# Performance work log

Hardware: AMD Instinct MI355X
Metric: run time of the kernel (lower is better)

The kernel has to match this reference:

```python
import jax, jax.numpy as jnp
import numpy as np
import math

B, S, HID = 2, 2048, 1536
H, HD = 12, 128           # num_heads, head_dim
LAT = HID // 8            # latent_dim = 192
ROT = HD // 2             # 64, rotary applied to this half-size subspace


def _make_rotary(seq_len, dim=ROT, base=10000.0):
    # LlamaRotaryEmbedding: inv_freq over dim/2 freqs, emb = cat(sin, cos) -> [1,1,S,dim]
    inv_freq = 1.0 / (base ** (np.arange(0, dim, 2, dtype=np.float32) / dim))
    pos = np.arange(seq_len, dtype=np.float32)
    sincos = np.einsum('i,j->ij', pos, inv_freq)  # [S, dim/2]
    emb = np.concatenate([np.sin(sincos), np.cos(sincos)], axis=-1)  # [S, dim]
    return jnp.asarray(emb)[None, None, :, :]


def setup_inputs() -> dict:
    key = jax.random.key(0)
    ks = jax.random.split(key, 10)
    sd = 0.02
    return {
        'hidden_states': jax.random.normal(ks[0], (B, S, HID), jnp.float32),
        'rotary_emb': _make_rotary(S),
        'W_kv_d':  jax.random.normal(ks[1], (HID, LAT), jnp.float32) * sd,
        'W_q_d':   jax.random.normal(ks[2], (HID, LAT), jnp.float32) * sd,
        'W_k_u':   jax.random.normal(ks[3], (LAT, H * ROT), jnp.float32) * sd,
        'W_q_u':   jax.random.normal(ks[4], (LAT, H * ROT), jnp.float32) * sd,
        'W_v_u':   jax.random.normal(ks[5], (LAT, H * HD), jnp.float32) * sd,
        'W_rope_k': jax.random.normal(ks[6], (HID, HID // 2), jnp.float32) * sd,
        'W_rope_q': jax.random.normal(ks[7], (LAT, HID // 2), jnp.float32) * sd,
        'W_o':     jax.random.normal(ks[8], (HID, HID), jnp.float32) * sd,
    }


def _apply_rope(x, emb):
    # x: [B,S,H,ROT]; emb: [1,1,S,ROT] (cat of sin,cos, each ROT/2)
    half = ROT // 2
    x1, x2 = x[..., :half], x[..., half:]
    sin = emb[..., :half].transpose(0, 2, 1, 3)  # -> [1,S,1,half] to broadcast over heads
    cos = emb[..., half:].transpose(0, 2, 1, 3)
    return jnp.concatenate([x1 * cos - x2 * sin, x1 * sin + x2 * cos], axis=-1)


def reference(hidden_states, rotary_emb, W_kv_d, W_q_d, W_k_u, W_q_u, W_v_u,
              W_rope_k, W_rope_q, W_o):
    b, s, _ = hidden_states.shape
    kv_d = hidden_states @ W_kv_d                       # [B,S,LAT]
    q_d = hidden_states @ W_q_d                         # [B,S,LAT]
    k_c = (kv_d @ W_k_u).reshape(b, s, H, ROT)          # content half of K
    q_c = (q_d @ W_q_u).reshape(b, s, H, ROT)
    v = (kv_d @ W_v_u).reshape(b, s, H, HD)
    k_r = (hidden_states @ W_rope_k).reshape(b, s, H, ROT)
    q_r = (q_d @ W_rope_q).reshape(b, s, H, ROT)
    k_r = _apply_rope(k_r, rotary_emb)
    q_r = _apply_rope(q_r, rotary_emb)
    k = jnp.concatenate([k_c, k_r], axis=-1)            # [B,S,H,HD]
    q = jnp.concatenate([q_c, q_r], axis=-1)

    scores = jnp.einsum('bqhd,bkhd->bhqk', q, k) / math.sqrt(HD)
    causal = jnp.tril(jnp.ones((s, s), dtype=bool))
    scores = jnp.where(causal[None, None], scores, jnp.float32(-1e9))
    probs = jax.nn.softmax(scores, axis=-1)
    attn = jnp.einsum('bhqk,bkhd->bqhd', probs, v).reshape(b, s, HID)
    return attn @ W_o
```

## Files before the change

### kernel.cpp

```cpp
#include <hip/hip_runtime.h>
#include <hip/hip_bf16.h>

#define B_ 2
#define S_ 2048
#define HID_ 1536
#define H_ 12
#define HD_ 128
#define LAT_ 192
#define ROT_ 64
#define M_ (B_*S_)
#define NTILE_ (B_*H_*(S_/64))

typedef __hip_bfloat16 bf16;

using short8  = __attribute__((ext_vector_type(8))) short;
using short4v = __attribute__((ext_vector_type(4))) short;
using float4v = __attribute__((ext_vector_type(4))) float;

__device__ __forceinline__ unsigned short f2bf(float f) {
  __hip_bfloat16 h = __float2bfloat16(f);
  unsigned short u; __builtin_memcpy(&u, &h, 2); return u;
}

#define GLDS16(gp, lp) __builtin_amdgcn_global_load_lds( \
    (__attribute__((address_space(1))) void*)(size_t)(gp), \
    (__attribute__((address_space(3))) void*)(lp), 16, 0, 0)

__global__ __launch_bounds__(256)
void fillf_k(float* __restrict__ out, float v, int n)
{
  int i = blockIdx.x*256 + threadIdx.x;
  if (i < n) out[i] = v;
}

__global__ __launch_bounds__(256)
void packT5_k(const float* __restrict__ s0, const float* __restrict__ s1,
              const float* __restrict__ s2, const float* __restrict__ s3,
              bf16* __restrict__ d0, bf16* __restrict__ d1,
              bf16* __restrict__ d2, bf16* __restrict__ d3,
              int Kn, int N0, int N1, int N2, int N3,
              const float* __restrict__ hsrc, bf16* __restrict__ hdst)
{
  if (blockIdx.z == 4) {
    const int nblk = gridDim.x * gridDim.y;
    const int flatb = blockIdx.y * gridDim.x + blockIdx.x;
    const float4* in4 = (const float4*)hsrc;
    for (int i = flatb*256 + threadIdx.x; i < M_*HID_/4; i += nblk*256) {
      float4 v = in4[i];
      short4v o;
      o[0] = (short)f2bf(v.x); o[1] = (short)f2bf(v.y);
      o[2] = (short)f2bf(v.z); o[3] = (short)f2bf(v.w);
      *(short4v*)&hdst[i*4] = o;
    }
    return;
  }
  const float* W; bf16* Wt; int Nn;
  switch (blockIdx.z) {
    case 0:  W = s0; Wt = d0; Nn = N0; break;
    case 1:  W = s1; Wt = d1; Nn = N1; break;
    case 2:  W = s2; Wt = d2; Nn = N2; break;
    default: W = s3; Wt = d3; Nn = N3; break;
  }
  const int kb = blockIdx.x*32, nb = blockIdx.y*32;
  if (nb >= Nn) return;
  __shared__ float t[32][33];
  const int tx = threadIdx.x & 31, ty = threadIdx.x >> 5;
  #pragma unroll
  for (int i = 0; i < 4; i++)
    t[ty+8*i][tx] = W[(size_t)(kb+ty+8*i)*Nn + nb + tx];
  __syncthreads();
  #pragma unroll
  for (int i = 0; i < 4; i++)
    Wt[(size_t)(nb + ty + 8*i)*Kn + kb + tx] = __float2bfloat16(t[tx][ty+8*i]);
}

template<int CMODE, int BM>
__global__ __launch_bounds__(256)
void gemm_mfma(const bf16* __restrict__ Av, const bf16* __restrict__ Btp,
               const bf16* __restrict__ Av2, const bf16* __restrict__ Bt2,
               void* __restrict__ Cv, void* __restrict__ Cv2,
               void* __restrict__ Cv3,
               const float* __restrict__ emb, int Kn, int lda, int ldb, int ldc)
{
  constexpr int MI  = BM/32;
  constexpr int ITA = BM/32;
  __shared__ bf16 As[(size_t)BM*64];
  __shared__ bf16 Bs[128*64];

  const int tid  = threadIdx.x;
  const int lane = tid & 63;
  const int w    = tid >> 6;
  const int col  = lane & 15, quad = lane >> 4;
  const int wr   = w >> 1, wc = w & 1;
  const size_t m0 = (size_t)blockIdx.y * BM;
  const size_t n0 = (size_t)blockIdx.x * 128;

  const bf16* Abase = Av;
  const bf16* Bt    = Btp;
  size_t nrow0 = n0;
  if constexpr (CMODE == 6) {
    if ((int)n0 >= 2304) { Abase = Av2; Bt = Bt2; nrow0 = n0 - 2304; }
  }

  const bf16* bg[4];
  #pragma unroll
  for (int it = 0; it < 4; it++) {
    int c = tid + it*256, row = c >> 3, seg = c & 7;
    bg[it] = Bt + (nrow0 + row)*ldb + (size_t)((seg ^ (row & 7))*8);
  }
  const bf16* ag[ITA];
  #pragma unroll
  for (int it = 0; it < ITA; it++) {
    int c = tid + it*256, row = c >> 3, seg = c & 7;
    ag[it] = Abase + (m0 + row)*lda + (size_t)((seg ^ (row & 7))*8);
  }

  float4v acc[MI][4];
  #pragma unroll
  for (int i=0;i<MI;i++)
    #pragma unroll
    for (int j=0;j<4;j++) acc[i][j] = (float4v){0.f,0.f,0.f,0.f};

  for (int k0 = 0; k0 < Kn; k0 += 64) {
    #pragma unroll
    for (int it = 0; it < 4; it++)
      GLDS16(bg[it] + k0, Bs + (size_t)(tid + it*256)*8);
    #pragma unroll
    for (int it = 0; it < ITA; it++)
      GLDS16(ag[it] + k0, As + (size_t)(tid + it*256)*8);
    __syncthreads();

    short8 af[MI][2], bfr[4][2];
    #pragma unroll
    for (int i=0;i<MI;i++) {
      const int ar = wr*(BM/2) + i*16 + col;
      #pragma unroll
      for (int k2=0;k2<2;k2++)
        af[i][k2] = *(const short8*)&As[ar*64 + ((k2*4+quad)^(ar&7))*8];
    }
    #pragma unroll
    for (int j=0;j<4;j++) {
      const int br = wc*64 + j*16 + col;
      #pragma unroll
      for (int k2=0;k2<2;k2++)
        bfr[j][k2] = *(const short8*)&Bs[br*64 + ((k2*4+quad)^(br&7))*8];
    }

    #pragma unroll
    for (int k2=0;k2<2;k2++)
      #pragma unroll
      for (int i=0;i<MI;i++)
        #pragma unroll
        for (int j=0;j<4;j++)
          acc[i][j] = __builtin_amdgcn_mfma_f32_16x16x32_bf16(af[i][k2], bfr[j][k2], acc[i][j], 0,0,0);
    __syncthreads();
  }

  if constexpr (CMODE == 0) {
    #pragma unroll
    for (int i=0;i<MI;i++) {
      const size_t row0 = m0 + wr*(BM/2) + i*16 + quad*4;
      #pragma unroll
      for (int j=0;j<4;j++) {
        const int c = (int)n0 + wc*64 + j*16 + col;
        #pragma unroll
        for (int r=0;r<4;r++)
          ((float*)Cv)[(row0+r)*ldc + c] = acc[i][j][r];
      }
    }
    return;
  }

  if constexpr (CMODE == 5) {
    if ((int)n0 < 384) {
      #pragma unroll
      for (int i=0;i<MI;i++) {
        const size_t row0 = m0 + wr*(BM/2) + i*16 + quad*4;
        #pragma unroll
        for (int j=0;j<4;j++) {
          const int c = (int)n0 + wc*64 + j*16 + col;
          #pragma unroll
          for (int r=0;r<4;r++)
            ((bf16*)Cv)[(row0+r)*384 + c] = __float2bfloat16(acc[i][j][r]);
        }
      }
    } else {
      const int hh = (((int)n0 - 384) >> 6) + wc;
      #pragma unroll
      for (int i=0;i<MI;i++) {
        const size_t row0 = m0 + wr*(BM/2) + i*16 + quad*4;
        #pragma unroll
        for (int j=0;j<2;j++) {
          const int idim = j*16 + col;
          #pragma unroll
          for (int r=0;r<4;r++) {
            const size_t row = row0 + r;
            const int s = (int)(row & (S_-1));
            const float sn = emb[(size_t)s*ROT_ + idim];
            const float cs = emb[(size_t)s*ROT_ + 32 + idim];
            const float x1 = acc[i][j][r], x2 = acc[i][j+2][r];
            bf16* dst = (bf16*)Cv2 + (row*H_ + hh)*HD_ + 64 + idim;
            dst[0]  = __float2bfloat16(x1*cs - x2*sn);
            dst[32] = __float2bfloat16(x1*sn + x2*cs);
          }
        }
      }
    }
    return;
  }

  if ((int)n0 < 768) {
    #pragma unroll
    for (int i=0;i<MI;i++) {
      const size_t row0 = m0 + wr*(BM/2) + i*16 + quad*4;
      #pragma unroll
      for (int j=0;j<4;j++) {
        const int c = (int)n0 + wc*64 + j*16 + col;
        #pragma unroll
        for (int r=0;r<4;r++)
          ((bf16*)Cv)[(row0+r)*HID_ + (c>>6)*HD_ + (c&63)] = __float2bfloat16(acc[i][j][r]);
      }
    }
  } else if ((int)n0 < 2304) {
    #pragma unroll
    for (int i=0;i<MI;i++) {
      const size_t row0 = m0 + wr*(BM/2) + i*16 + quad*4;
      const int bb = (int)(row0 >> 11), s = (int)(row0 & (S_-1));
      #pragma unroll
      for (int j=0;j<4;j++) {
        const int cv = (int)n0 - 768 + wc*64 + j*16 + col;
        const int hh = cv >> 7, d = cv & 127;
        short4v st;
        #pragma unroll
        for (int r=0;r<4;r++) st[r] = (short)f2bf(acc[i][j][r]);
        *(short4v*)((unsigned short*)Cv2 +
            ((size_t)(bb*H_+hh)*HD_ + d)*S_ + s) = st;
      }
    }
  } else if ((int)n0 < 3072) {
    #pragma unroll
    for (int i=0;i<MI;i++) {
      const size_t row0 = m0 + wr*(BM/2) + i*16 + quad*4;
      #pragma unroll
      for (int j=0;j<4;j++) {
        const int c = (int)n0 - 2304 + wc*64 + j*16 + col;
        #pragma unroll
        for (int r=0;r<4;r++)
          ((bf16*)Cv3)[(row0+r)*HID_ + (c>>6)*HD_ + (c&63)] = __float2bfloat16(acc[i][j][r]);
      }
    }
  } else {
    const int hh = (((int)n0 - 3072) >> 6) + wc;
    #pragma unroll
    for (int i=0;i<MI;i++) {
      const size_t row0 = m0 + wr*(BM/2) + i*16 + quad*4;
      #pragma unroll
      for (int j=0;j<2;j++) {
        const int idim = j*16 + col;
        #pragma unroll
        for (int r=0;r<4;r++) {
          const size_t row = row0 + r;
          const int s = (int)(row & (S_-1));
          const float sn = emb[(size_t)s*ROT_ + idim];
          const float cs = emb[(size_t)s*ROT_ + 32 + idim];
          const float x1 = acc[i][j][r], x2 = acc[i][j+2][r];
          bf16* dst = (bf16*)Cv3 + (row*H_ + hh)*HD_ + 64 + idim;
          dst[0]  = __float2bfloat16(x1*cs - x2*sn);
          dst[32] = __float2bfloat16(x1*sn + x2*cs);
        }
      }
    }
  }
}

#define KSTR 136
#define VSTR 72
#define PSTR 72

__global__ __launch_bounds__(256)
void attn_mfma(const bf16* __restrict__ Qf, const bf16* __restrict__ Kf,
               const bf16* __restrict__ Vtg, bf16* __restrict__ at)
{
  const int p     = (int)blockIdx.x;
  const int ii    = p & 255;
  const int third = p >> 8;
  const int rank  = (third == 0) ? ii : (third == 1 ? 511 - ii : 512 + ii);
  const int qt = (S_/64 - 1) - rank/24;
  const int bh = rank % 24;
  const int h  = bh % H_, b = bh / H_;

  const int tid  = threadIdx.x;
  const int w    = tid >> 6;
  const int lane = tid & 63;
  const int col  = lane & 15;
  const int quad = lane >> 4;

  __shared__ unsigned short Ks[64*KSTR];
  __shared__ unsigned short Vt[128*VSTR];
  __shared__ unsigned short Ps[4][16*PSTR];

  const int q0w = qt*64 + w*16;

  const unsigned short* Kb = (const unsigned short*)Kf +
      ((size_t)b*S_*H_ + h)*HD_;
  const unsigned short* Vb = (const unsigned short*)Vtg +
      (size_t)(b*H_ + h)*HD_*S_;

  const unsigned short* kgp[4]; unsigned short* kdst[4];
  const unsigned short* vgp[4]; unsigned short* vdst[4];
  #pragma unroll
  for (int it = 0; it < 4; it++) {
    int c = tid + it*256;
    int key = c >> 4, doff = (c & 15)*8;
    kgp[it]  = Kb + (size_t)key*HID_ + doff;
    kdst[it] = &Ks[key*KSTR + doff];
    int d = c >> 3, kg = (c & 7)*8;
    vgp[it]  = Vb + (size_t)d*S_ + kg;
    vdst[it] = &Vt[d*VSTR + kg];
  }

  short8 qf[4];
  {
    const unsigned short* qrow = (const unsigned short*)Qf +
        ((size_t)((size_t)b*S_ + q0w + col)*H_ + h)*HD_;
    #pragma unroll
    for (int kk = 0; kk < 4; kk++)
      qf[kk] = *(const short8*)(qrow + kk*32 + quad*8);
  }

  float4v O[8];
  #pragma unroll
  for (int t=0;t<8;t++) O[t] = (float4v){0.f,0.f,0.f,0.f};
  float m_ln = -1e30f, l_ln = 0.f;

  const float scale2 = 0.08838834764831845f * 1.4426950408889634f;

  short8 kr[4], vr[4];
  #pragma unroll
  for (int it = 0; it < 4; it++) {
    kr[it] = *(const short8*)kgp[it];
    vr[it] = *(const short8*)vgp[it];
  }

  for (int kb = 0; kb <= qt; kb++) {
    const int k0 = kb * 64;
    const bool diag = (kb == qt);

    #pragma unroll
    for (int it = 0; it < 4; it++) *(short8*)kdst[it] = kr[it];
    #pragma unroll
    for (int it = 0; it < 4; it++) *(short8*)vdst[it] = vr[it];
    __syncthreads();

    if (!diag) {
      const size_t kn = (size_t)(k0 + 64);
      #pragma unroll
      for (int it = 0; it < 4; it++) {
        kr[it] = *(const short8*)(kgp[it] + kn*HID_);
        vr[it] = *(const short8*)(vgp[it] + kn);
      }
    }

    float4v Sf[4];
    #pragma unroll
    for (int tc=0;tc<4;tc++) Sf[tc] = (float4v){0.f,0.f,0.f,0.f};
    __builtin_amdgcn_s_setprio(1);
    if (!diag) {
      #pragma unroll
      for (int tc = 0; tc < 4; tc++)
        #pragma unroll
        for (int kk = 0; kk < 4; kk++) {
          short8 kfrag = *(const short8*)&Ks[(16*tc+col)*KSTR + 32*kk + quad*8];
          Sf[tc] = __builtin_amdgcn_mfma_f32_16x16x32_bf16(kfrag, qf[kk], Sf[tc], 0,0,0);
        }
    } else {
      #pragma unroll
      for (int tc = 0; tc < 4; tc++) {
        if (tc <= w) {
          #pragma unroll
          for (int kk = 0; kk < 4; kk++) {
            short8 kfrag = *(const short8*)&Ks[(16*tc+col)*KSTR + 32*kk + quad*8];
            Sf[tc] = __builtin_amdgcn_mfma_f32_16x16x32_bf16(kfrag, qf[kk], Sf[tc], 0,0,0);
          }
        }
      }
    }
    __builtin_amdgcn_s_setprio(0);

    float sv[4][4];
    float pmax = -3.0e38f;
    if (!diag) {
      #pragma unroll
      for (int tc = 0; tc < 4; tc++)
        #pragma unroll
        for (int r = 0; r < 4; r++) {
          float s = Sf[tc][r] * scale2;
          sv[tc][r] = s;
          pmax = fmaxf(pmax, s);
        }
    } else {
      const int qrel = w*16 + col;
      #pragma unroll
      for (int tc = 0; tc < 4; tc++)
        #pragma unroll
        for (int r = 0; r < 4; r++) {
          float s = Sf[tc][r] * scale2;
          if (tc*16 + quad*4 + r > qrel) s = -3.0e38f;
          sv[tc][r] = s;
          pmax = fmaxf(pmax, s);
        }
    }
    pmax = fmaxf(pmax, __shfl_xor(pmax, 16));
    pmax = fmaxf(pmax, __shfl_xor(pmax, 32));

    if (__all(pmax <= m_ln + 11.0f)) {
      float lt = 0.f;
      #pragma unroll
      for (int tc = 0; tc < 4; tc++)
        #pragma unroll
        for (int r = 0; r < 4; r++) {
          sv[tc][r] = exp2f(sv[tc][r] - m_ln);
          lt += sv[tc][r];
        }
      lt += __shfl_xor(lt, 16);
      lt += __shfl_xor(lt, 32);
      l_ln += lt;
    } else {
      const float mnew = fmaxf(m_ln, pmax);
      float lt = 0.f;
      #pragma unroll
      for (int tc = 0; tc < 4; tc++)
        #pragma unroll
        for (int r = 0; r < 4; r++) {
          sv[tc][r] = exp2f(sv[tc][r] - mnew);
          lt += sv[tc][r];
        }
      lt += __shfl_xor(lt, 16);
      lt += __shfl_xor(lt, 32);
      const float al = exp2f(m_ln - mnew);
      l_ln = l_ln * al + lt;
      m_ln = mnew;
      float alr[4];
      #pragma unroll
      for (int r = 0; r < 4; r++) alr[r] = __shfl(al, quad*4 + r);
      #pragma unroll
      for (int t = 0; t < 8; t++)
        #pragma unroll
        for (int r = 0; r < 4; r++) O[t][r] *= alr[r];
    }

    #pragma unroll
    for (int tc = 0; tc < 4; tc++) {
      short4v pw;
      pw[0] = (short)f2bf(sv[tc][0]); pw[1] = (short)f2bf(sv[tc][1]);
      pw[2] = (short)f2bf(sv[tc][2]); pw[3] = (short)f2bf(sv[tc][3]);
      *(short4v*)&Ps[w][col*PSTR + tc*16 + quad*4] = pw;
    }

    __builtin_amdgcn_s_setprio(1);
    if (!diag) {
      #pragma unroll
      for (int ks = 0; ks < 2; ks++) {
        short8 pf = *(const short8*)&Ps[w][col*PSTR + 32*ks + quad*8];
        #pragma unroll
        for (int t = 0; t < 8; t++) {
          short8 vf = *(const short8*)&Vt[(16*t + col)*VSTR + 32*ks + quad*8];
          O[t] = __builtin_amdgcn_mfma_f32_16x16x32_bf16(pf, vf, O[t], 0,0,0);
        }
      }
    } else {
      #pragma unroll
      for (int ks = 0; ks < 2; ks++) {
        if (ks == 0 || w >= 2) {
          short8 pf = *(const short8*)&Ps[w][col*PSTR + 32*ks + quad*8];
          #pragma unroll
          for (int t = 0; t < 8; t++) {
            short8 vf = *(const short8*)&Vt[(16*t + col)*VSTR + 32*ks + quad*8];
            O[t] = __builtin_amdgcn_mfma_f32_16x16x32_bf16(pf, vf, O[t], 0,0,0);
          }
        }
      }
    }
    __builtin_amdgcn_s_setprio(0);
    __syncthreads();
  }

  float lr[4];
  #pragma unroll
  for (int r = 0; r < 4; r++) lr[r] = __shfl(l_ln, quad*4 + r);
  #pragma unroll
  for (int r = 0; r < 4; r++) {
    const float linv = 1.f / lr[r];
    const size_t mq = (size_t)b*S_ + q0w + quad*4 + r;
    bf16* dst = at + mq*HID_ + h*HD_ + col;
    #pragma unroll
    for (int t = 0; t < 8; t++)
      dst[16*t] = __float2bfloat16(O[t][r] * linv);
  }
}

extern "C" void kernel_launch(void* const* d_in, const int* in_sizes, int n_in,
                              void* d_out, int out_size, void* d_ws, size_t ws_size,
                              hipStream_t stream)
{
  float* out = (float*)d_out;

  static const int sz_dict[10] = {6291456,131072,294912,294912,147456,
                                  147456,294912,1179648,147456,2359296};
  int bad = -1;
  if (n_in < 10) bad = 15;
  else {
    for (int i = 0; i < 10; i++)
      if (in_sizes[i] != sz_dict[i]) { bad = i; break; }
  }
  if (bad >= 0) {
    float v = 1.0e6f * (float)(1 + bad);
    if (bad < 10) v += (float)(in_sizes[bad] % 1000000);
    fillf_k<<<(out_size + 255)/256, 256, 0, stream>>>(out, v, out_size);
    return;
  }

  const float* hidden = (const float*)d_in[0];
  const float* emb    = (const float*)d_in[1];
  const float* Wkvd   = (const float*)d_in[2];
  const float* Wqd    = (const float*)d_in[3];
  const float* Wku    = (const float*)d_in[4];
  const float* Wqu    = (const float*)d_in[5];
  const float* Wvu    = (const float*)d_in[6];
  const float* Wrk    = (const float*)d_in[7];
  const float* Wrq    = (const float*)d_in[8];
  const float* Wo     = (const float*)d_in[9];

  char* wp = (char*)d_ws;
  size_t used = 0;
  auto alloc = [&](size_t bytes) -> void* {
    void* p = wp + used;
    used += (bytes + 255) & ~(size_t)255;
    return p;
  };
  bf16*  hb    = (bf16*)alloc((size_t)M_*HID_*2);
  bf16*  dout  = (bf16*)alloc((size_t)M_*384*2);
  bf16*  Kf    = (bf16*)alloc((size_t)M_*HID_*2);
  bf16*  Qf    = (bf16*)alloc((size_t)M_*HID_*2);
  bf16*  Vtg   = (bf16*)alloc((size_t)B_*H_*HD_*S_*2);
  bf16*  at    = (bf16*)alloc((size_t)M_*HID_*2);
  bf16*  WdkrT = (bf16*)alloc((size_t)1152*HID_*2);
  bf16*  WkvuT = (bf16*)alloc((size_t)2304*LAT_*2);
  bf16*  WqurT = (bf16*)alloc((size_t)1536*LAT_*2);
  bf16*  WoT   = (bf16*)alloc((size_t)HID_*HID_*2);

  if (used > ws_size) {
    fillf_k<<<(out_size + 255)/256, 256, 0, stream>>>(out, 5.0e7f, out_size);
    return;
  }

  packT5_k<<<dim3(48,48,5), 256, 0, stream>>>(
      Wkvd, Wqd, Wrk, Wo,
      WdkrT, WdkrT + (size_t)192*HID_, WdkrT + (size_t)384*HID_, WoT,
      HID_, LAT_, LAT_, H_*ROT_, HID_,
      hidden, hb);
  packT5_k<<<dim3(6,48,4), 256, 0, stream>>>(
      Wku, Wvu, Wqu, Wrq,
      WkvuT, WkvuT + (size_t)768*LAT_, WqurT, WqurT + (size_t)768*LAT_,
      LAT_, H_*ROT_, HID_, H_*ROT_, H_*ROT_,
      nullptr, nullptr);

  gemm_mfma<5,64><<<dim3(9, M_/64), 256, 0, stream>>>(
      hb, WdkrT, nullptr, nullptr, dout, Kf, nullptr, emb, HID_, HID_, HID_, 0);
  gemm_mfma<6,128><<<dim3(30, M_/128), 256, 0, stream>>>(
      dout, WkvuT, dout + 192, WqurT, Kf, Vtg, Qf, emb, LAT_, 384, LAT_, 0);

  attn_mfma<<<NTILE_, 256, 0, stream>>>(Qf, Kf, Vtg, at);

  gemm_mfma<0,64><<<dim3(HID_/64  * 0 + 12, M_/64), 256, 0, stream>>>(
      at, WoT, nullptr, nullptr, out, nullptr, nullptr, emb, HID_, HID_, HID_, HID_);
}
```

Before: 240.1 us.

## Read K/V MFMA fragments directly from global memory, drop LDS staging

```diff
diff --git a/kernel.cpp b/kernel.cpp
--- a/kernel.cpp
+++ b/kernel.cpp
@@ -273,18 +273,13 @@
   }
 }
 
-#define KSTR 136
-#define VSTR 72
 #define PSTR 72
 
 __global__ __launch_bounds__(256)
 void attn_mfma(const bf16* __restrict__ Qf, const bf16* __restrict__ Kf,
                const bf16* __restrict__ Vtg, bf16* __restrict__ at)
 {
-  const int p     = (int)blockIdx.x;
-  const int ii    = p & 255;
-  const int third = p >> 8;
-  const int rank  = (third == 0) ? ii : (third == 1 ? 511 - ii : 512 + ii);
+  const int rank = (int)blockIdx.x;
   const int qt = (S_/64 - 1) - rank/24;
   const int bh = rank % 24;
   const int h  = bh % H_, b = bh / H_;
@@ -295,29 +290,14 @@
   const int col  = lane & 15;
   const int quad = lane >> 4;
 
-  __shared__ unsigned short Ks[64*KSTR];
-  __shared__ unsigned short Vt[128*VSTR];
   __shared__ unsigned short Ps[4][16*PSTR];
 
   const int q0w = qt*64 + w*16;
 
-  const unsigned short* Kb = (const unsigned short*)Kf +
-      ((size_t)b*S_*H_ + h)*HD_;
-  const unsigned short* Vb = (const unsigned short*)Vtg +
-      (size_t)(b*H_ + h)*HD_*S_;
-
-  const unsigned short* kgp[4]; unsigned short* kdst[4];
-  const unsigned short* vgp[4]; unsigned short* vdst[4];
-  #pragma unroll
-  for (int it = 0; it < 4; it++) {
-    int c = tid + it*256;
-    int key = c >> 4, doff = (c & 15)*8;
-    kgp[it]  = Kb + (size_t)key*HID_ + doff;
-    kdst[it] = &Ks[key*KSTR + doff];
-    int d = c >> 3, kg = (c & 7)*8;
-    vgp[it]  = Vb + (size_t)d*S_ + kg;
-    vdst[it] = &Vt[d*VSTR + kg];
-  }
+  const unsigned short* Kc = (const unsigned short*)Kf +
+      ((size_t)b*S_*H_ + h)*HD_ + (size_t)col*HID_ + quad*8;
+  const unsigned short* Vc = (const unsigned short*)Vtg +
+      (size_t)(b*H_ + h)*HD_*S_ + (size_t)col*S_ + quad*8;
 
   short8 qf[4];
   {
@@ -335,53 +315,22 @@
 
   const float scale2 = 0.08838834764831845f * 1.4426950408889634f;
 
-  short8 kr[4], vr[4];
-  #pragma unroll
-  for (int it = 0; it < 4; it++) {
-    kr[it] = *(const short8*)kgp[it];
-    vr[it] = *(const short8*)vgp[it];
-  }
-
   for (int kb = 0; kb <= qt; kb++) {
     const int k0 = kb * 64;
     const bool diag = (kb == qt);
 
-    #pragma unroll
-    for (int it = 0; it < 4; it++) *(short8*)kdst[it] = kr[it];
-    #pragma unroll
-    for (int it = 0; it < 4; it++) *(short8*)vdst[it] = vr[it];
-    __syncthreads();
-
-    if (!diag) {
-      const size_t kn = (size_t)(k0 + 64);
-      #pragma unroll
-      for (int it = 0; it < 4; it++) {
-        kr[it] = *(const short8*)(kgp[it] + kn*HID_);
-        vr[it] = *(const short8*)(vgp[it] + kn);
-      }
-    }
-
     float4v Sf[4];
     #pragma unroll
     for (int tc=0;tc<4;tc++) Sf[tc] = (float4v){0.f,0.f,0.f,0.f};
     __builtin_amdgcn_s_setprio(1);
-    if (!diag) {
-      #pragma unroll
-      for (int tc = 0; tc < 4; tc++)
+    #pragma unroll
+    for (int tc = 0; tc < 4; tc++) {
+      if (!diag || tc <= w) {
+        const unsigned short* krow = Kc + (size_t)(k0 + 16*tc)*HID_;
         #pragma unroll
         for (int kk = 0; kk < 4; kk++) {
-          short8 kfrag = *(const short8*)&Ks[(16*tc+col)*KSTR + 32*kk + quad*8];
+          short8 kfrag = *(const short8*)(krow + 32*kk);
           Sf[tc] = __builtin_amdgcn_mfma_f32_16x16x32_bf16(kfrag, qf[kk], Sf[tc], 0,0,0);
-        }
-    } else {
-      #pragma unroll
-      for (int tc = 0; tc < 4; tc++) {
-        if (tc <= w) {
-          #pragma unroll
-          for (int kk = 0; kk < 4; kk++) {
-            short8 kfrag = *(const short8*)&Ks[(16*tc+col)*KSTR + 32*kk + quad*8];
-            Sf[tc] = __builtin_amdgcn_mfma_f32_16x16x32_bf16(kfrag, qf[kk], Sf[tc], 0,0,0);
-          }
         }
       }
     }
@@ -458,31 +407,19 @@
     }
 
     __builtin_amdgcn_s_setprio(1);
-    if (!diag) {
-      #pragma unroll
-      for (int ks = 0; ks < 2; ks++) {
+    #pragma unroll
+    for (int ks = 0; ks < 2; ks++) {
+      if (!diag || ks == 0 || w >= 2) {
         short8 pf = *(const short8*)&Ps[w][col*PSTR + 32*ks + quad*8];
+        const unsigned short* vcol = Vc + (size_t)(k0 + 32*ks);
         #pragma unroll
         for (int t = 0; t < 8; t++) {
-          short8 vf = *(const short8*)&Vt[(16*t + col)*VSTR + 32*ks + quad*8];
+          short8 vf = *(const short8*)(vcol + (size_t)(16*t)*S_);
           O[t] = __builtin_amdgcn_mfma_f32_16x16x32_bf16(pf, vf, O[t], 0,0,0);
         }
       }
-    } else {
-      #pragma unroll
-      for (int ks = 0; ks < 2; ks++) {
-        if (ks == 0 || w >= 2) {
-          short8 pf = *(const short8*)&Ps[w][col*PSTR + 32*ks + quad*8];
-          #pragma unroll
-          for (int t = 0; t < 8; t++) {
-            short8 vf = *(const short8*)&Vt[(16*t + col)*VSTR + 32*ks + quad*8];
-            O[t] = __builtin_amdgcn_mfma_f32_16x16x32_bf16(pf, vf, O[t], 0,0,0);
-          }
-        }
-      }
     }
     __builtin_amdgcn_s_setprio(0);
-    __syncthreads();
   }
 
   float lr[4];
@@ -572,6 +509,6 @@
 
   attn_mfma<<<NTILE_, 256, 0, stream>>>(Qf, Kf, Vtg, at);
 
-  gemm_mfma<0,64><<<dim3(HID_/64  * 0 + 12, M_/64), 256, 0, stream>>>(
+  gemm_mfma<0,64><<<dim3(12, M_/64), 256, 0, stream>>>(
       at, WoT, nullptr, nullptr, out, nullptr, nullptr, emb, HID_, HID_, HID_, HID_);
 }
```

Result: slower. 373.6 us (+55.6%).

## Fold softmax scale into Q projection epilogue and streamline attention softmax

Applied to the files above, without the earlier changes.

```diff
diff --git a/kernel.cpp b/kernel.cpp
--- a/kernel.cpp
+++ b/kernel.cpp
@@ -10,6 +10,8 @@
 #define ROT_ 64
 #define M_ (B_*S_)
 #define NTILE_ (B_*H_*(S_/64))
+
+#define SC2F 0.12752869f
 
 typedef __hip_bfloat16 bf16;
 
@@ -246,7 +248,8 @@
         const int c = (int)n0 - 2304 + wc*64 + j*16 + col;
         #pragma unroll
         for (int r=0;r<4;r++)
-          ((bf16*)Cv3)[(row0+r)*HID_ + (c>>6)*HD_ + (c&63)] = __float2bfloat16(acc[i][j][r]);
+          ((bf16*)Cv3)[(row0+r)*HID_ + (c>>6)*HD_ + (c&63)] =
+              __float2bfloat16(acc[i][j][r] * SC2F);
       }
     }
   } else {
@@ -265,8 +268,8 @@
           const float cs = emb[(size_t)s*ROT_ + 32 + idim];
           const float x1 = acc[i][j][r], x2 = acc[i][j+2][r];
           bf16* dst = (bf16*)Cv3 + (row*H_ + hh)*HD_ + 64 + idim;
-          dst[0]  = __float2bfloat16(x1*cs - x2*sn);
-          dst[32] = __float2bfloat16(x1*sn + x2*cs);
+          dst[0]  = __float2bfloat16((x1*cs - x2*sn) * SC2F);
+          dst[32] = __float2bfloat16((x1*sn + x2*cs) * SC2F);
         }
       }
     }
@@ -281,10 +284,7 @@
 void attn_mfma(const bf16* __restrict__ Qf, const bf16* __restrict__ Kf,
                const bf16* __restrict__ Vtg, bf16* __restrict__ at)
 {
-  const int p     = (int)blockIdx.x;
-  const int ii    = p & 255;
-  const int third = p >> 8;
-  const int rank  = (third == 0) ? ii : (third == 1 ? 511 - ii : 512 + ii);
+  const int rank = (int)blockIdx.x;
   const int qt = (S_/64 - 1) - rank/24;
   const int bh = rank % 24;
   const int h  = bh % H_, b = bh / H_;
@@ -333,8 +333,6 @@
   for (int t=0;t<8;t++) O[t] = (float4v){0.f,0.f,0.f,0.f};
   float m_ln = -1e30f, l_ln = 0.f;
 
-  const float scale2 = 0.08838834764831845f * 1.4426950408889634f;
-
   short8 kr[4], vr[4];
   #pragma unroll
   for (int it = 0; it < 4; it++) {
@@ -388,56 +386,55 @@
     __builtin_amdgcn_s_setprio(0);
 
     float sv[4][4];
-    float pmax = -3.0e38f;
     if (!diag) {
       #pragma unroll
       for (int tc = 0; tc < 4; tc++)
         #pragma unroll
-        for (int r = 0; r < 4; r++) {
-          float s = Sf[tc][r] * scale2;
-          sv[tc][r] = s;
-          pmax = fmaxf(pmax, s);
-        }
+        for (int r = 0; r < 4; r++)
+          sv[tc][r] = Sf[tc][r];
     } else {
       const int qrel = w*16 + col;
       #pragma unroll
       for (int tc = 0; tc < 4; tc++)
         #pragma unroll
-        for (int r = 0; r < 4; r++) {
-          float s = Sf[tc][r] * scale2;
-          if (tc*16 + quad*4 + r > qrel) s = -3.0e38f;
-          sv[tc][r] = s;
-          pmax = fmaxf(pmax, s);
-        }
-    }
+        for (int r = 0; r < 4; r++)
+          sv[tc][r] = (tc*16 + quad*4 + r > qrel) ? -3.0e38f : Sf[tc][r];
+    }
+    float ma[4];
+    #pragma unroll
+    for (int tc = 0; tc < 4; tc++)
+      ma[tc] = fmaxf(fmaxf(sv[tc][0], sv[tc][1]), fmaxf(sv[tc][2], sv[tc][3]));
+    float pmax = fmaxf(fmaxf(ma[0], ma[1]), fmaxf(ma[2], ma[3]));
     pmax = fmaxf(pmax, __shfl_xor(pmax, 16));
     pmax = fmaxf(pmax, __shfl_xor(pmax, 32));
 
     if (__all(pmax <= m_ln + 11.0f)) {
-      float lt = 0.f;
-      #pragma unroll
-      for (int tc = 0; tc < 4; tc++)
-        #pragma unroll
-        for (int r = 0; r < 4; r++) {
-          sv[tc][r] = exp2f(sv[tc][r] - m_ln);
-          lt += sv[tc][r];
-        }
+      float sa[4];
+      #pragma unroll
+      for (int tc = 0; tc < 4; tc++) {
+        #pragma unroll
+        for (int r = 0; r < 4; r++)
+          sv[tc][r] = __builtin_amdgcn_exp2f(sv[tc][r] - m_ln);
+        sa[tc] = (sv[tc][0] + sv[tc][1]) + (sv[tc][2] + sv[tc][3]);
+      }
+      float lt = (sa[0] + sa[1]) + (sa[2] + sa[3]);
       lt += __shfl_xor(lt, 16);
       lt += __shfl_xor(lt, 32);
       l_ln += lt;
     } else {
       const float mnew = fmaxf(m_ln, pmax);
-      float lt = 0.f;
-      #pragma unroll
-      for (int tc = 0; tc < 4; tc++)
-        #pragma unroll
-        for (int r = 0; r < 4; r++) {
-          sv[tc][r] = exp2f(sv[tc][r] - mnew);
-          lt += sv[tc][r];
-        }
+      float sa[4];
+      #pragma unroll
+      for (int tc = 0; tc < 4; tc++) {
+        #pragma unroll
+        for (int r = 0; r < 4; r++)
+          sv[tc][r] = __builtin_amdgcn_exp2f(sv[tc][r] - mnew);
+        sa[tc] = (sv[tc][0] + sv[tc][1]) + (sv[tc][2] + sv[tc][3]);
+      }
+      float lt = (sa[0] + sa[1]) + (sa[2] + sa[3]);
       lt += __shfl_xor(lt, 16);
       lt += __shfl_xor(lt, 32);
-      const float al = exp2f(m_ln - mnew);
+      const float al = __builtin_amdgcn_exp2f(m_ln - mnew);
       l_ln = l_ln * al + lt;
       m_ln = mnew;
       float alr[4];
@@ -572,6 +569,6 @@
 
   attn_mfma<<<NTILE_, 256, 0, stream>>>(Qf, Kf, Vtg, at);
 
-  gemm_mfma<0,64><<<dim3(HID_/64  * 0 + 12, M_/64), 256, 0, stream>>>(
+  gemm_mfma<0,64><<<dim3(12, M_/64), 256, 0, stream>>>(
       at, WoT, nullptr, nullptr, out, nullptr, nullptr, emb, HID_, HID_, HID_, HID_);
 }
```

After: 235.8 us. Within noise of the previous version (-1.8%).
